# Performance work log

Measured on AMD Instinct MI355X. Metric: run time of the kernel, lower is better.

## Reference

```python
import jax, jax.numpy as jnp
import numpy as np

B, T, M, H = 64, 256, 512, 256  # batch, seq_len, d_model, lstm hidden


def setup_inputs() -> dict:
    key = jax.random.key(0)
    ks = jax.random.split(key, 10)
    s = 0.05  # weight init scale
    return {
        "enc_inputs": jax.random.normal(ks[0], (B, T, M), jnp.float32),
        "y": jax.random.normal(ks[1], (B, T, 1), jnp.float32),
        "Wd_w": jax.random.normal(ks[2], (M, 2 * H), jnp.float32) * s,  # W_d: Linear(2H, M)
        "Wd_b": jnp.zeros((M,), jnp.float32),
        "Ud_w": jax.random.normal(ks[3], (M, M), jnp.float32) * s,      # U_d: Linear(M, M, bias=False)
        "vd_w": jax.random.normal(ks[4], (1, M), jnp.float32) * s,      # v_d: Linear(M, 1, bias=False)
        "wt_w": jax.random.normal(ks[5], (1, M + 1), jnp.float32) * s,  # w_tilda: Linear(M+1, 1)
        "wt_b": jnp.zeros((1,), jnp.float32),
        "Wih": jax.random.normal(ks[6], (4 * H, 1), jnp.float32) * s,   # LSTMCell input weights
        "Whh": jax.random.normal(ks[7], (4 * H, H), jnp.float32) * s,   # LSTMCell hidden weights
        "bih": jnp.zeros((4 * H,), jnp.float32),
        "bhh": jnp.zeros((4 * H,), jnp.float32),
    }


def reference(enc_inputs, y, Wd_w, Wd_b, Ud_w, vd_w, wt_w, wt_b, Wih, Whh, bih, bhh):
    # U_d(enc_inputs) is loop-invariant -> hoist (same math as recomputing each step)
    y1 = jnp.einsum('btm,nm->btn', enc_inputs, Ud_w)  # [B,T,M]

    def step(carry, y_t):
        d, s = carry  # d = h_{t-1} [B,H], s = c'_{t-1} [B,H]
        x1 = jnp.concatenate([d, s], axis=1) @ Wd_w.T + Wd_b          # [B,M]
        z1 = jnp.tanh(x1[:, None, :] + y1)                            # [B,T,M]
        l_it = jnp.einsum('btm,m->bt', z1, vd_w[0])                   # [B,T]
        beta = jax.nn.softmax(l_it, axis=1)                           # softmax over encoder steps
        c_t = jnp.einsum('bt,btm->bm', beta, enc_inputs)              # [B,M]
        y_tilda = jnp.concatenate([c_t, y_t], axis=1) @ wt_w.T + wt_b # [B,1]
        # torch LSTMCell: gate order i, f, g, o
        gates = y_tilda @ Wih.T + bih + d @ Whh.T + bhh               # [B,4H]
        i, f, g, o = jnp.split(gates, 4, axis=1)
        s_new = jax.nn.sigmoid(f) * s + jax.nn.sigmoid(i) * jnp.tanh(g)
        d_new = jax.nn.sigmoid(o) * jnp.tanh(s_new)
        return (d_new, s_new), c_t

    b = enc_inputs.shape[0]
    init = (jnp.zeros((b, H), enc_inputs.dtype), jnp.zeros((b, H), enc_inputs.dtype))
    _, cs = jax.lax.scan(step, init, jnp.swapaxes(y, 0, 1))  # cs: [T,B,M]
    return jnp.sum(cs, axis=0)  # tgt = sum_t c_t, [B,M]
```

## Files before the change

### kernel.cpp

```cpp
#include <hip/hip_runtime.h>

typedef unsigned short u16;
typedef unsigned int u32;
typedef __attribute__((ext_vector_type(8))) short short8v;
typedef __attribute__((ext_vector_type(4))) float f32x4;
typedef __attribute__((ext_vector_type(4))) unsigned int u32x4;

#define NB 64
#define NT 256
#define NM 512
#define NH 256

#define K2 2.8853900817779268f
#define LOG2E 1.4426950408889634f

__device__ __forceinline__ float bf2f(u16 u) {
  union { unsigned i; float f; } c; c.i = ((unsigned)u) << 16; return c.f;
}
__device__ __forceinline__ u16 f2bf(float f) {
  union { float fv; unsigned i; } c; c.fv = f;
  unsigned i = c.i;
  return (u16)((i + 0x7fffu + ((i >> 16) & 1u)) >> 16);
}
__device__ __forceinline__ float bits2f(u32 u) {
  union { unsigned i; float f; } c; c.i = u; return c.f;
}
__device__ __forceinline__ float tanh_fast(float x) {
  return 1.0f - 2.0f * __builtin_amdgcn_rcpf(1.0f + __builtin_amdgcn_exp2f(K2 * x));
}
__device__ __forceinline__ float sigmoid_fast(float x) {
  return __builtin_amdgcn_rcpf(1.0f + __builtin_amdgcn_exp2f(-LOG2E * x));
}

__device__ __forceinline__ float unc_ld1(const float* p) {
  float r;
  asm volatile("global_load_dword %0, %1, off sc0 sc1\n\ts_waitcnt vmcnt(0)"
               : "=&v"(r) : "v"(p) : "memory");
  return r;
}
__device__ __forceinline__ void unc_ld1x4(const float* p0, const float* p1,
                                          const float* p2, const float* p3,
                                          float& a0, float& a1, float& a2, float& a3) {
  asm volatile(
      "global_load_dword %0, %4, off sc0 sc1\n\t"
      "global_load_dword %1, %5, off sc0 sc1\n\t"
      "global_load_dword %2, %6, off sc0 sc1\n\t"
      "global_load_dword %3, %7, off sc0 sc1\n\t"
      "s_waitcnt vmcnt(0)"
      : "=&v"(a0), "=&v"(a1), "=&v"(a2), "=&v"(a3)
      : "v"(p0), "v"(p1), "v"(p2), "v"(p3)
      : "memory");
}
__device__ __forceinline__ f32x4 unc_ld4f(const float* p) {
  f32x4 r;
  asm volatile("global_load_dwordx4 %0, %1, off sc0 sc1\n\ts_waitcnt vmcnt(0)"
               : "=&v"(r) : "v"(p) : "memory");
  return r;
}
__device__ __forceinline__ void unc_st1(float* p, float v) {
  asm volatile("global_store_dword %0, %1, off sc0 sc1" :: "v"(p), "v"(v) : "memory");
}
__device__ __forceinline__ void unc_st1u(u32* p, u32 v) {
  asm volatile("global_store_dword %0, %1, off sc0 sc1" :: "v"(p), "v"(v) : "memory");
}
__device__ __forceinline__ void unc_st4(float* p, f32x4 v) {
  asm volatile("global_store_dwordx4 %0, %1, off sc0 sc1" :: "v"(p), "v"(v) : "memory");
}
__device__ __forceinline__ void drain_vmem() {
  asm volatile("s_waitcnt vmcnt(0)" ::: "memory");
}
__device__ __forceinline__ void pollflags(const u32* p, u32 tg) {
  for (;;) {
    u32x4 f;
    asm volatile("global_load_dwordx4 %0, %1, off sc0 sc1\n\ts_waitcnt vmcnt(0)"
                 : "=&v"(f) : "v"(p) : "memory");
    if (f[0] >= tg && f[1] >= tg && f[2] >= tg && f[3] >= tg) break;
    __builtin_amdgcn_s_sleep(1);
  }
}

__global__ void convert_f32_bf16(const float* __restrict__ in, u16* __restrict__ out, int n) {
  int i = blockIdx.x * blockDim.x + threadIdx.x;
  if (i < n) out[i] = f2bf(in[i]);
}

__global__ __launch_bounds__(256) void gemm_y1(const u16* __restrict__ A,
                                               const u16* __restrict__ Bm,
                                               u16* __restrict__ C) {
  const int w = threadIdx.x >> 6;
  const int l = threadIdx.x & 63;
  const int kg = l >> 4;
  const int r16 = l & 15;
  const int rowbase = blockIdx.x * 64 + w * 16;
  const int colbase = blockIdx.y * 64;
  const u16* ap = A + (size_t)(rowbase + r16) * 512 + kg * 8;
  f32x4 acc0 = {0,0,0,0}, acc1 = {0,0,0,0}, acc2 = {0,0,0,0}, acc3 = {0,0,0,0};
  for (int k = 0; k < 512; k += 32) {
    short8v af = *(const short8v*)(ap + k);
    const u16* bp = Bm + (size_t)(colbase + r16) * 512 + kg * 8 + k;
    short8v b0 = *(const short8v*)(bp);
    short8v b1 = *(const short8v*)(bp + 16 * 512);
    short8v b2 = *(const short8v*)(bp + 32 * 512);
    short8v b3 = *(const short8v*)(bp + 48 * 512);
    acc0 = __builtin_amdgcn_mfma_f32_16x16x32_bf16(af, b0, acc0, 0, 0, 0);
    acc1 = __builtin_amdgcn_mfma_f32_16x16x32_bf16(af, b1, acc1, 0, 0, 0);
    acc2 = __builtin_amdgcn_mfma_f32_16x16x32_bf16(af, b2, acc2, 0, 0, 0);
    acc3 = __builtin_amdgcn_mfma_f32_16x16x32_bf16(af, b3, acc3, 0, 0, 0);
  }
  #pragma unroll
  for (int j = 0; j < 4; ++j) {
    int r = rowbase + (l >> 4) * 4 + j;
    C[(size_t)r * 512 + colbase +  0 + r16] = f2bf(K2 * acc0[j]);
    C[(size_t)r * 512 + colbase + 16 + r16] = f2bf(K2 * acc1[j]);
    C[(size_t)r * 512 + colbase + 32 + r16] = f2bf(K2 * acc2[j]);
    C[(size_t)r * 512 + colbase + 48 + r16] = f2bf(K2 * acc3[j]);
  }
}

__global__ __launch_bounds__(256) void wenc_kernel(const u16* __restrict__ encbf,
                                                   const float* __restrict__ wtw,
                                                   float* __restrict__ gwenc) {
  int b = blockIdx.x, te = threadIdx.x;
  const u16* ep = encbf + ((size_t)(b * NT + te)) * NM;
  float a = 0.0f;
  for (int c8 = 0; c8 < 64; ++c8) {
    short8v v = *(const short8v*)(ep + c8 * 8);
    #pragma unroll
    for (int jj = 0; jj < 8; ++jj) a = fmaf(bf2f((u16)v[jj]), wtw[c8 * 8 + jj], a);
  }
  gwenc[b * NT + te] = a;
}

__global__ __launch_bounds__(1024, 1) void attn_scan(
    const u16* __restrict__ y1bf,
    const u16* __restrict__ encbf,
    const u16* __restrict__ whhbf,
    const u16* __restrict__ wdbf,
    const float* __restrict__ Wd_b,
    const float* __restrict__ vd,
    const float* __restrict__ wtw,
    const float* __restrict__ wtb,
    const float* __restrict__ Wih,
    const float* __restrict__ bih,
    const float* __restrict__ bhh,
    const float* __restrict__ yin,
    const float* __restrict__ gwenc,
    float* __restrict__ gx,
    float* __restrict__ st,
    u32* __restrict__ flags,
    float* __restrict__ out)
{
  extern __shared__ char ldsraw[];
  u32* wdsl = (u32*)ldsraw;

  __shared__ float x1_l[NM];
  __shared__ float d_l[NH];
  __shared__ float ds_f[128];
  __shared__ float l_sl[64];
  __shared__ float e_sl[64];
  __shared__ float whh_d_l[256];
  __shared__ float wih_l[256];
  __shared__ float bb_l[256];
  __shared__ float wdb_l[NM];
  __shared__ float wenc_sl[64];
  __shared__ float ct_red[NM];

  const int tid = threadIdx.x;
  const int bid = blockIdx.x;
  const int xcd = bid & 7, ii = bid >> 3;
  const int b = (xcd << 3) | (ii >> 2);
  const int q = ii & 3;
  const int w = tid >> 6, l = tid & 63;

  if (tid < 512) wdb_l[tid] = Wd_b[tid];
  if (tid < 256) {
    int g = tid >> 6, h = tid & 63;
    int r = g * 256 + q * 64 + h;
    wih_l[tid] = Wih[r];
    bb_l[tid] = bih[r] + bhh[r];
  }
  if (tid < 64) wenc_sl[tid] = gwenc[b * NT + q * 64 + tid];
  float vr[8];
  #pragma unroll
  for (int j = 0; j < 8; ++j) vr[j] = vd[l + 64 * j];
  float sv = 0.0f;
  #pragma unroll
  for (int j = 0; j < 8; ++j) sv += vr[j];
  #pragma unroll
  for (int off = 32; off > 0; off >>= 1) sv += __shfl_xor(sv, off, 64);
  const float Svd = sv;
  const float wtw512 = wtw[NM];
  const float wtb0 = wtb[0];

  {
    int m = tid >> 1, kh = tid & 1;
    for (int j = 0; j < 32; ++j) {
      int p = kh * 32 + j;
      int k0 = 2 * p, k1 = 2 * p + 1;
      int c0 = (k0 < 64) ? q * 64 + k0 : 256 + q * 64 + (k0 - 64);
      int c1 = (k1 < 64) ? q * 64 + k1 : 256 + q * 64 + (k1 - 64);
      u32 lo = wdbf[m * 512 + c0];
      u32 hi = wdbf[m * 512 + c1];
      int g = p >> 2, pg = g ^ (m & 15);
      wdsl[m * 64 + pg * 4 + (p & 3)] = lo | (hi << 16);
    }
  }

  float s_reg = 0.0f;
  float out_acc = 0.0f;
  __syncthreads();

  float* gxb = gx + b * 2304;
  float* stb = st + b * 16;
  u32* fS = flags + b * 32;
  u32* fP = flags + b * 32 + 8;

  #pragma unroll 1
  for (int t = 0; t < NT; ++t) {
    pollflags(fP, (u32)t);
    if (tid < 512) {
      const float* p = gxb + tid;
      float a0, a1, a2, a3;
      unc_ld1x4(p, p + 576, p + 1152, p + 1728, a0, a1, a2, a3);
      x1_l[tid] = K2 * (wdb_l[tid] + ((a0 + a1) + (a2 + a3)));
    } else if (tid < 768) {
      int h = tid - 512;
      d_l[h] = unc_ld1(gxb + (h >> 6) * 576 + 512 + (h & 63));
    }
    __syncthreads();

    float x1r[8];
    #pragma unroll
    for (int j = 0; j < 8; ++j) x1r[j] = x1_l[l + 64 * j];
    {
      const u16* yrow = y1bf + ((size_t)(b * NT + q * 64 + w * 4) << 9);
      #pragma unroll
      for (int i = 0; i < 4; ++i) {
        float a = 0.0f;
        #pragma unroll
        for (int j = 0; j < 8; ++j) {
          float yv = bf2f(yrow[i * 512 + l + 64 * j]);
          float e = __builtin_amdgcn_exp2f(x1r[j] + yv);
          a = fmaf(vr[j], __builtin_amdgcn_rcpf(1.0f + e), a);
        }
        #pragma unroll
        for (int off = 32; off > 0; off >>= 1) a += __shfl_xor(a, off, 64);
        if (l == i) l_sl[w * 4 + i] = Svd - 2.0f * a;
      }
    }
    __syncthreads();

    if (w == 0) {
      float v = l_sl[l];
      float mq = v;
      #pragma unroll
      for (int off = 32; off > 0; off >>= 1) mq = fmaxf(mq, __shfl_xor(mq, off, 64));
      float e = __builtin_amdgcn_exp2f((v - mq) * LOG2E);
      e_sl[l] = e;
      float sq = e, nq = e * wenc_sl[l];
      #pragma unroll
      for (int off = 32; off > 0; off >>= 1) {
        sq += __shfl_xor(sq, off, 64);
        nq += __shfl_xor(nq, off, 64);
      }
      if (l == 0) {
        f32x4 quad = {mq, sq, nq, 0.0f};
        unc_st4(stb + q * 4, quad);
        drain_vmem();
        unc_st1u(fS + q, (u32)(t + 1));
      }
    } else {
      #pragma unroll 1
      for (int pass = 0; pass < 2; ++pass) {
        int slot = (pass == 0) ? (tid - 64) : (tid - 64 + 960);
        if (pass == 1 && tid >= 128) break;
        int rl = slot >> 2, kq = slot & 3;
        const u16* wr = whhbf + (size_t)((rl >> 6) * 256 + q * 64 + (rl & 63)) * 256 + kq * 64;
        float a = 0.0f;
        #pragma unroll
        for (int c8 = 0; c8 < 8; ++c8) {
          short8v wv = *(const short8v*)(wr + c8 * 8);
          #pragma unroll
          for (int jj = 0; jj < 8; ++jj)
            a = fmaf(bf2f((u16)wv[jj]), d_l[kq * 64 + c8 * 8 + jj], a);
        }
        a += __shfl_xor(a, 1, 64);
        a += __shfl_xor(a, 2, 64);
        if (kq == 0) whh_d_l[rl] = a;
      }
    }

    pollflags(fS, (u32)(t + 1));
    f32x4 s0 = unc_ld4f(stb + 0);
    f32x4 s1 = unc_ld4f(stb + 4);
    f32x4 s2 = unc_ld4f(stb + 8);
    f32x4 s3 = unc_ld4f(stb + 12);
    float mx = fmaxf(fmaxf(s0[0], s1[0]), fmaxf(s2[0], s3[0]));
    float w0 = __builtin_amdgcn_exp2f((s0[0] - mx) * LOG2E);
    float w1 = __builtin_amdgcn_exp2f((s1[0] - mx) * LOG2E);
    float w2 = __builtin_amdgcn_exp2f((s2[0] - mx) * LOG2E);
    float w3 = __builtin_amdgcn_exp2f((s3[0] - mx) * LOG2E);
    float den = fmaf(s0[1], w0, fmaf(s1[1], w1, fmaf(s2[1], w2, s3[1] * w3)));
    float rden = __builtin_amdgcn_rcpf(den);
    float nsum = fmaf(s0[2], w0, fmaf(s1[2], w1, fmaf(s2[2], w2, s3[2] * w3)));
    float yt = nsum * rden + wtw512 * yin[b * NT + t] + wtb0;
    float wq = (q == 0) ? w0 : (q == 1) ? w1 : (q == 2) ? w2 : w3;
    float sc_q = wq * rden;
    __syncthreads();

    if (tid < 64) {
      int h = tid;
      float gi = sigmoid_fast(whh_d_l[h]       + yt * wih_l[h]       + bb_l[h]);
      float gf = sigmoid_fast(whh_d_l[64 + h]  + yt * wih_l[64 + h]  + bb_l[64 + h]);
      float gg = tanh_fast   (whh_d_l[128 + h] + yt * wih_l[128 + h] + bb_l[128 + h]);
      float go = sigmoid_fast(whh_d_l[192 + h] + yt * wih_l[192 + h] + bb_l[192 + h]);
      float sn = gf * s_reg + gi * gg;
      s_reg = sn;
      float dn = go * tanh_fast(sn);
      ds_f[h] = dn;
      ds_f[64 + h] = sn;
      unc_st1(gxb + q * 576 + 512 + h, dn);
    }
    __syncthreads();

    {
      int m = tid >> 1, kh = tid & 1;
      float a = 0.0f;
      #pragma unroll
      for (int i = 0; i < 8; ++i) {
        int g = kh * 8 + i, pg = g ^ (m & 15);
        u32x4 wv = *(const u32x4*)(wdsl + m * 64 + pg * 4);
        const f32x4 dv0 = *(const f32x4*)(ds_f + kh * 64 + i * 8);
        const f32x4 dv1 = *(const f32x4*)(ds_f + kh * 64 + i * 8 + 4);
        #pragma unroll
        for (int n = 0; n < 4; ++n) {
          u32 v = wv[n];
          float wlo = bits2f(v << 16);
          float whi = bits2f(v & 0xffff0000u);
          float dlo = (n < 2) ? dv0[2 * n] : dv1[2 * n - 4];
          float dhi = (n < 2) ? dv0[2 * n + 1] : dv1[2 * n - 3];
          a = fmaf(wlo, dlo, a);
          a = fmaf(whi, dhi, a);
        }
      }
      a += __shfl_xor(a, 1, 64);
      if (kh == 0) unc_st1(gxb + q * 576 + m, a);
    }
    drain_vmem();
    __syncthreads();
    if (tid == 0) unc_st1u(fP + q, (u32)(t + 1));

    {
      int c = tid >> 9, m = tid & 511;
      const u16* ep = encbf + ((size_t)(b * NT + q * 64 + c * 32) << 9) + m;
      float a = 0.0f;
      #pragma unroll 8
      for (int i = 0; i < 32; ++i)
        a = fmaf(bf2f(ep[(size_t)i * 512]), e_sl[c * 32 + i], a);
      if (c) ct_red[m] = a;
      __syncthreads();
      if (!c) out_acc += (a + ct_red[m]) * sc_q;
    }
  }

  if (tid < 512)
    __hip_atomic_fetch_add(&out[b * NM + tid], out_acc,
                           __ATOMIC_RELAXED, __HIP_MEMORY_SCOPE_SYSTEM);
}

extern "C" void kernel_launch(void* const* d_in, const int* in_sizes, int n_in,
                              void* d_out, int out_size, void* d_ws, size_t ws_size,
                              hipStream_t stream) {
  const float* enc  = (const float*)d_in[0];
  const float* yin  = (const float*)d_in[1];
  const float* Wd_w = (const float*)d_in[2];
  const float* Wd_b = (const float*)d_in[3];
  const float* Ud_w = (const float*)d_in[4];
  const float* vd_w = (const float*)d_in[5];
  const float* wt_w = (const float*)d_in[6];
  const float* wt_b = (const float*)d_in[7];
  const float* Wih  = (const float*)d_in[8];
  const float* Whh  = (const float*)d_in[9];
  const float* bih  = (const float*)d_in[10];
  const float* bhh  = (const float*)d_in[11];

  char* ws = (char*)d_ws;
  u16*   y1bf  = (u16*)(ws);
  u16*   encbf = (u16*)(ws + 16777216);
  u16*   udbf  = (u16*)(ws + 33554432);
  u16*   wdbf  = (u16*)(ws + 34078720);
  u16*   whhbf = (u16*)(ws + 34603008);
  float* gwenc = (float*)(ws + 35127296);
  float* gx    = (float*)(ws + 35192832);
  float* st    = (float*)(ws + 35782656);
  u32*   flags = (u32*)(ws + 35786752);

  hipMemsetAsync(ws + 35192832, 0, 602112, stream);
  hipMemsetAsync(d_out, 0, (size_t)out_size * sizeof(float), stream);

  convert_f32_bf16<<<8388608 / 256, 256, 0, stream>>>(enc, encbf, 8388608);
  convert_f32_bf16<<<262144 / 256, 256, 0, stream>>>(Ud_w, udbf, 262144);
  convert_f32_bf16<<<262144 / 256, 256, 0, stream>>>(Wd_w, wdbf, 262144);
  convert_f32_bf16<<<262144 / 256, 256, 0, stream>>>(Whh, whhbf, 262144);
  gemm_y1<<<dim3(256, 8), 256, 0, stream>>>(encbf, udbf, y1bf);
  wenc_kernel<<<64, 256, 0, stream>>>(encbf, wt_w, gwenc);

  hipFuncSetAttribute((const void*)attn_scan,
                      hipFuncAttributeMaxDynamicSharedMemorySize, 131072);
  attn_scan<<<256, 1024, 131072, stream>>>(y1bf, encbf, whhbf, wdbf, Wd_b, vd_w,
                                           wt_w, wt_b, Wih, bih, bhh, yin, gwenc,
                                           gx, st, flags, (float*)d_out);
}
```

Before: 4.420 ms.

## Keep y1 and encoder slices in registers and overlap context accumulation

Each block now loads its y1 rows and encoder rows into registers once before the time loop, instead of re-reading them from global memory every step. The column mapping changes to contiguous 8-element chunks per lane. The context-vector accumulation moves to waves 8-15 and runs concurrently with the LSTM gate update, with one atomic flush at the end. The Wd matvec is reassigned to waves 0-7 with one row per thread, dropping the shuffle reduce. The extra resident registers raise register pressure, and launch bounds are changed to a min-blocks value of 4.

```diff
diff --git a/kernel.cpp b/kernel.cpp
--- a/kernel.cpp
+++ b/kernel.cpp
@@ -51,11 +51,16 @@
       : "v"(p0), "v"(p1), "v"(p2), "v"(p3)
       : "memory");
 }
-__device__ __forceinline__ f32x4 unc_ld4f(const float* p) {
-  f32x4 r;
-  asm volatile("global_load_dwordx4 %0, %1, off sc0 sc1\n\ts_waitcnt vmcnt(0)"
-               : "=&v"(r) : "v"(p) : "memory");
-  return r;
+__device__ __forceinline__ void unc_ld16f(const float* p, f32x4& a, f32x4& b,
+                                          f32x4& c, f32x4& d) {
+  asm volatile(
+      "global_load_dwordx4 %0, %4, off sc0 sc1\n\t"
+      "global_load_dwordx4 %1, %4, off offset:16 sc0 sc1\n\t"
+      "global_load_dwordx4 %2, %4, off offset:32 sc0 sc1\n\t"
+      "global_load_dwordx4 %3, %4, off offset:48 sc0 sc1\n\t"
+      "s_waitcnt vmcnt(0)"
+      : "=&v"(a), "=&v"(b), "=&v"(c), "=&v"(d)
+      : "v"(p) : "memory");
 }
 __device__ __forceinline__ void unc_st1(float* p, float v) {
   asm volatile("global_store_dword %0, %1, off sc0 sc1" :: "v"(p), "v"(v) : "memory");
@@ -131,7 +136,7 @@
   gwenc[b * NT + te] = a;
 }
 
-__global__ __launch_bounds__(1024, 1) void attn_scan(
+__global__ __launch_bounds__(1024, 4) void attn_scan(
     const u16* __restrict__ y1bf,
     const u16* __restrict__ encbf,
     const u16* __restrict__ whhbf,
@@ -163,7 +168,6 @@
   __shared__ float bb_l[256];
   __shared__ float wdb_l[NM];
   __shared__ float wenc_sl[64];
-  __shared__ float ct_red[NM];
 
   const int tid = threadIdx.x;
   const int bid = blockIdx.x;
@@ -180,9 +184,10 @@
     bb_l[tid] = bih[r] + bhh[r];
   }
   if (tid < 64) wenc_sl[tid] = gwenc[b * NT + q * 64 + tid];
+
   float vr[8];
   #pragma unroll
-  for (int j = 0; j < 8; ++j) vr[j] = vd[l + 64 * j];
+  for (int j = 0; j < 8; ++j) vr[j] = vd[l * 8 + j];
   float sv = 0.0f;
   #pragma unroll
   for (int j = 0; j < 8; ++j) sv += vr[j];
@@ -191,6 +196,19 @@
   const float Svd = sv;
   const float wtw512 = wtw[NM];
   const float wtb0 = wtb[0];
+
+  short8v y1R[4];
+  #pragma unroll
+  for (int i = 0; i < 4; ++i)
+    y1R[i] = *(const short8v*)(y1bf + ((size_t)(b * NT + q * 64 + w * 4 + i) << 9) + l * 8);
+  const int w8 = w - 8;
+  short8v encR[8];
+  if (w >= 8) {
+    #pragma unroll
+    for (int i = 0; i < 8; ++i)
+      encR[i] = *(const short8v*)(encbf + ((size_t)(b * NT + q * 64 + w8 * 8 + i) << 9) + l * 8);
+  }
+  float ctacc[8] = {0,0,0,0,0,0,0,0};
 
   {
     int m = tid >> 1, kh = tid & 1;
@@ -207,7 +225,6 @@
   }
 
   float s_reg = 0.0f;
-  float out_acc = 0.0f;
   __syncthreads();
 
   float* gxb = gx + b * 2304;
@@ -229,23 +246,21 @@
     }
     __syncthreads();
 
-    float x1r[8];
-    #pragma unroll
-    for (int j = 0; j < 8; ++j) x1r[j] = x1_l[l + 64 * j];
     {
-      const u16* yrow = y1bf + ((size_t)(b * NT + q * 64 + w * 4) << 9);
+      const f32x4 x0 = *(const f32x4*)(x1_l + l * 8);
+      const f32x4 x1v = *(const f32x4*)(x1_l + l * 8 + 4);
+      float xr[8] = {x0[0], x0[1], x0[2], x0[3], x1v[0], x1v[1], x1v[2], x1v[3]};
       #pragma unroll
       for (int i = 0; i < 4; ++i) {
         float a = 0.0f;
         #pragma unroll
         for (int j = 0; j < 8; ++j) {
-          float yv = bf2f(yrow[i * 512 + l + 64 * j]);
-          float e = __builtin_amdgcn_exp2f(x1r[j] + yv);
+          float e = __builtin_amdgcn_exp2f(xr[j] + bf2f((u16)y1R[i][j]));
           a = fmaf(vr[j], __builtin_amdgcn_rcpf(1.0f + e), a);
         }
         #pragma unroll
         for (int off = 32; off > 0; off >>= 1) a += __shfl_xor(a, off, 64);
-        if (l == i) l_sl[w * 4 + i] = Svd - 2.0f * a;
+        if (l == 0) l_sl[w * 4 + i] = Svd - 2.0f * a;
       }
     }
     __syncthreads();
@@ -291,10 +306,8 @@
     }
 
     pollflags(fS, (u32)(t + 1));
-    f32x4 s0 = unc_ld4f(stb + 0);
-    f32x4 s1 = unc_ld4f(stb + 4);
-    f32x4 s2 = unc_ld4f(stb + 8);
-    f32x4 s3 = unc_ld4f(stb + 12);
+    f32x4 s0, s1, s2, s3;
+    unc_ld16f(stb, s0, s1, s2, s3);
     float mx = fmaxf(fmaxf(s0[0], s1[0]), fmaxf(s2[0], s3[0]));
     float w0 = __builtin_amdgcn_exp2f((s0[0] - mx) * LOG2E);
     float w1 = __builtin_amdgcn_exp2f((s1[0] - mx) * LOG2E);
@@ -320,52 +333,54 @@
       ds_f[h] = dn;
       ds_f[64 + h] = sn;
       unc_st1(gxb + q * 576 + 512 + h, dn);
+    } else if (w >= 8) {
+      float tmp[8] = {0,0,0,0,0,0,0,0};
+      #pragma unroll
+      for (int i = 0; i < 8; ++i) {
+        float e = e_sl[w8 * 8 + i];
+        #pragma unroll
+        for (int j = 0; j < 8; ++j)
+          tmp[j] = fmaf(bf2f((u16)encR[i][j]), e, tmp[j]);
+      }
+      #pragma unroll
+      for (int j = 0; j < 8; ++j) ctacc[j] = fmaf(sc_q, tmp[j], ctacc[j]);
     }
     __syncthreads();
 
-    {
-      int m = tid >> 1, kh = tid & 1;
+    if (w < 8) {
+      int m = w * 64 + l;
+      const u32* row = wdsl + m * 64;
+      const int sw = (m & 15) << 2;
       float a = 0.0f;
       #pragma unroll
-      for (int i = 0; i < 8; ++i) {
-        int g = kh * 8 + i, pg = g ^ (m & 15);
-        u32x4 wv = *(const u32x4*)(wdsl + m * 64 + pg * 4);
-        const f32x4 dv0 = *(const f32x4*)(ds_f + kh * 64 + i * 8);
-        const f32x4 dv1 = *(const f32x4*)(ds_f + kh * 64 + i * 8 + 4);
+      for (int g = 0; g < 16; ++g) {
+        u32x4 wv = *(const u32x4*)(row + (((g << 2) ^ sw)));
+        f32x4 d0 = *(const f32x4*)(ds_f + g * 8);
+        f32x4 d1 = *(const f32x4*)(ds_f + g * 8 + 4);
         #pragma unroll
         for (int n = 0; n < 4; ++n) {
           u32 v = wv[n];
           float wlo = bits2f(v << 16);
           float whi = bits2f(v & 0xffff0000u);
-          float dlo = (n < 2) ? dv0[2 * n] : dv1[2 * n - 4];
-          float dhi = (n < 2) ? dv0[2 * n + 1] : dv1[2 * n - 3];
+          float dlo = (n < 2) ? d0[2 * n] : d1[2 * n - 4];
+          float dhi = (n < 2) ? d0[2 * n + 1] : d1[2 * n - 3];
           a = fmaf(wlo, dlo, a);
           a = fmaf(whi, dhi, a);
         }
       }
-      a += __shfl_xor(a, 1, 64);
-      if (kh == 0) unc_st1(gxb + q * 576 + m, a);
+      unc_st1(gxb + q * 576 + m, a);
     }
     drain_vmem();
     __syncthreads();
     if (tid == 0) unc_st1u(fP + q, (u32)(t + 1));
-
-    {
-      int c = tid >> 9, m = tid & 511;
-      const u16* ep = encbf + ((size_t)(b * NT + q * 64 + c * 32) << 9) + m;
-      float a = 0.0f;
-      #pragma unroll 8
-      for (int i = 0; i < 32; ++i)
-        a = fmaf(bf2f(ep[(size_t)i * 512]), e_sl[c * 32 + i], a);
-      if (c) ct_red[m] = a;
-      __syncthreads();
-      if (!c) out_acc += (a + ct_red[m]) * sc_q;
-    }
-  }
-
-  if (tid < 512)
-    __hip_atomic_fetch_add(&out[b * NM + tid], out_acc,
-                           __ATOMIC_RELAXED, __HIP_MEMORY_SCOPE_SYSTEM);
+  }
+
+  if (w >= 8) {
+    #pragma unroll
+    for (int j = 0; j < 8; ++j)
+      __hip_atomic_fetch_add(&out[b * NM + l * 8 + j], ctacc[j],
+                             __ATOMIC_RELAXED, __HIP_MEMORY_SCOPE_SYSTEM);
+  }
 }
 
 extern "C" void kernel_launch(void* const* d_in, const int* in_sizes, int n_in,
```

Result: slower. 6.175 ms (+39.7%).
